# Kernel optimization log

Hardware: AMD Instinct MI355X
Metric: run time of the kernel (lower is better)

The kernel has to match this reference:

```python
import jax, jax.numpy as jnp
import numpy as np

GRID_SIZE = 8
POS_LAMBDA = 250.0
POS_MARGIN = 1.0
NEG_MARGIN = 0.2


def setup_inputs() -> dict:
    key = jax.random.key(0)
    k1, k2, k3, k4 = jax.random.split(key, 4)
    N, C, Hr, Wr = 8, 128, 30, 40
    H, W = Hr * GRID_SIZE, Wr * GRID_SIZE
    des1 = jax.random.normal(k1, (N, C, Hr, Wr), jnp.float32)
    des2 = jax.random.normal(k2, (N, C, Hr, Wr), jnp.float32)
    # near-identity homography so the positive-pair mask s is non-trivial
    homo = jnp.eye(3, dtype=jnp.float32) + 0.001 * jax.random.normal(k3, (3, 3), jnp.float32)
    mask = (jax.random.uniform(k4, (N, 1, H, W)) > 0.05).astype(jnp.float32)
    return {"des1": des1, "des2": des2, "homo": homo, "mask": mask}


def reference(des1, des2, homo, mask):
    n, c, hr, wr = des1.shape
    gs = GRID_SIZE

    # coordinate grid of cell centers in full-res pixel coords: (x, y)
    ys, xs = jnp.meshgrid(jnp.arange(hr), jnp.arange(wr), indexing='ij')
    grid = jnp.stack([xs, ys], axis=-1).astype(homo.dtype) * gs + gs // 2  # Hr,Wr,2
    grid = jnp.broadcast_to(grid, (n, hr, wr, 2))

    # warp grid by homography
    gh = jnp.concatenate([grid, jnp.ones((n, hr, wr, 1), homo.dtype)], axis=-1)  # N,Hr,Wr,3
    wg = jnp.einsum('nhwk,jk->nhwj', gh, homo)
    w_grid = wg[..., :2] / wg[..., 2:3]  # N,Hr,Wr,2

    # pairwise distance between grid cells of img1 and warped cells of img2
    diff = grid[:, :, :, None, None, :] - w_grid[:, None, None, :, :, :]  # N,Hr,Wr,Hr,Wr,2
    grid_dist = jnp.sqrt(jnp.sum(diff * diff, axis=-1))                   # N,Hr,Wr,Hr,Wr
    s = (grid_dist <= gs - 0.5).astype(des1.dtype)

    # dense descriptor cross-correlation (contraction over channels)
    dot_des = jnp.einsum('ncij,nckl->nijkl', des1, des2)  # N,Hr,Wr,Hr,Wr

    pos_dist = jnp.maximum(POS_MARGIN - dot_des, 0.0)
    neg_dist = jnp.maximum(dot_des - NEG_MARGIN, 0.0)
    loss = POS_LAMBDA * s * pos_dist + (1.0 - s) * neg_dist

    # space_to_depth(mask, gs).prod(dim=1)
    m = mask.reshape(n, 1, hr, gs, wr, gs)
    r_mask = jnp.prod(m, axis=(1, 3, 5))            # N,Hr,Wr
    r_mask5 = r_mask.reshape(n, 1, 1, hr, wr)

    norm = hr * wr * jnp.sum(r_mask5)
    loss = jnp.sum(loss * r_mask5) / norm
    return (loss, s, dot_des, r_mask5[:, 0])  # r_mask squeezed -> N,1,Hr,Wr
```

## Files before the change

kernel.cpp:

```cpp
#include <hip/hip_runtime.h>
#include <hip/hip_bf16.h>

#define HRr 30
#define WRr 40
#define MM 1200
#define CC 128
#define NB 8
#define GS 8

constexpr int PT = 19;
constexpr int TILE_SH = 16 * 64 * 8;
constexpr int NPART = 1200;

typedef __attribute__((ext_vector_type(8))) short bf16x8;
typedef __attribute__((ext_vector_type(4))) float f32x4;

__device__ inline short f2bf(float f) {
    union { float f; unsigned u; } v; v.f = f;
    unsigned r = v.u + 0x7FFFu + ((v.u >> 16) & 1u);
    return (short)(r >> 16);
}

__global__ __launch_bounds__(256) void convert_prep_kernel(const float* __restrict__ des1,
                                                           const float* __restrict__ des2,
                                                           const float* __restrict__ homo,
                                                           const float* __restrict__ mask,
                                                           short* __restrict__ wsA,
                                                           short* __restrict__ wsB,
                                                           float2* __restrict__ wgrid,
                                                           float* __restrict__ out_rmask,
                                                           float* __restrict__ ws_rmask) {
    const int t     = threadIdx.x;
    const int ptile = blockIdx.x;
    const int n     = blockIdx.z;

    if (blockIdx.y == 0) {
        const int gid = (blockIdx.z * gridDim.x + blockIdx.x) * 256 + t;
        if (gid < MM) {
            int k = gid / WRr, l = gid % WRr;
            float x = (float)(l * GS + GS / 2);
            float y = (float)(k * GS + GS / 2);
            float nx = homo[0] * x + homo[1] * y + homo[2];
            float ny = homo[3] * x + homo[4] * y + homo[5];
            float dn = homo[6] * x + homo[7] * y + homo[8];
            wgrid[gid] = make_float2(nx / dn, ny / dn);
        }
        if (gid < NB * MM) {
            int nn = gid / MM;
            int rem = gid % MM;
            int k = rem / WRr, l = rem % WRr;
            const float* mp = mask + (size_t)nn * (240 * 320) + (size_t)(k * GS) * 320 + l * GS;
            float prod = 1.f;
            #pragma unroll
            for (int yy = 0; yy < GS; ++yy) {
                float4 a = *reinterpret_cast<const float4*>(&mp[yy * 320]);
                float4 b = *reinterpret_cast<const float4*>(&mp[yy * 320 + 4]);
                prod *= a.x * a.y * a.z * a.w * b.x * b.y * b.z * b.w;
            }
            out_rmask[gid] = prod;
            ws_rmask[gid]  = prod;
        }
    }

    const int j = t & 63;
    const int g = t >> 6;
    const int p = ptile * 64 + j;

    const float* A = des1 + (size_t)n * CC * MM;
    const float* B = des2 + (size_t)n * CC * MM;
    short* outA = wsA + (size_t)(n * PT + ptile) * TILE_SH;
    short* outB = wsB + (size_t)(n * PT + ptile) * TILE_SH;

    const int rb = j >> 4, lc = j & 15;
    const int kr = blockIdx.y * 4 + g;
    const int kb = kr * 8;
    bf16x8 wa, wb;
    #pragma unroll
    for (int i = 0; i < 8; ++i) {
        float va = (p < MM) ? A[(size_t)(kb + i) * MM + p] : 0.f;
        float vb = (p < MM) ? B[(size_t)(kb + i) * MM + p] : 0.f;
        wa[i] = f2bf(va);
        wb[i] = f2bf(vb);
    }
    const int ks = kr >> 2, lr = kr & 3;
    const size_t off = (size_t)(((ks * 4 + rb) * 64) + lr * 16 + lc) * 8;
    *reinterpret_cast<bf16x8*>(&outA[off]) = wa;
    *reinterpret_cast<bf16x8*>(&outB[off]) = wb;
}

__global__ __launch_bounds__(256) void main_kernel(const short* __restrict__ wsA,
                                                   const short* __restrict__ wsB,
                                                   const float2* __restrict__ wgrid,
                                                   const float* __restrict__ rmask,
                                                   float* __restrict__ out_s,
                                                   float* __restrict__ out_dot,
                                                   float* __restrict__ partials) {
    __shared__ float Ds[16 * 612];
    __shared__ float red[4];

    const int f   = blockIdx.x;
    const int lid = (f & 7) * 150 + (f >> 3);
    const int n     = lid / 150;
    const int rem   = lid % 150;
    const int strip = rem >> 1;
    const int half  = rem & 1;
    const int p0    = strip * 16;
    const int cbase = half ? 608 : 0;
    const int nf    = half ? 37  : 38;
    const int W     = half ? 592 : 608;
    const int fbase = half ? 38  : 0;

    const int t    = threadIdx.x;
    const int lane = t & 63;
    const int w    = t >> 6;
    const int lr   = lane >> 4, lc = lane & 15;

    const short* An  = wsA + (size_t)(n * PT + (p0 >> 6)) * TILE_SH;
    const int    rbA = (p0 >> 4) & 3;
    bf16x8 af[4];
    #pragma unroll
    for (int ks = 0; ks < 4; ++ks)
        af[ks] = *reinterpret_cast<const bf16x8*>(&An[(size_t)(((ks * 4 + rbA) * 64) + lane) * 8]);

    const short* Bn = wsB + (size_t)n * PT * TILE_SH;
    const float* rm = rmask + n * MM;

    for (int i = w; i < nf; i += 4) {
        const int g = fbase + i;
        const short* Bt = Bn + (size_t)(g >> 2) * TILE_SH;
        const int rbB = g & 3;
        f32x4 acc = {0.f, 0.f, 0.f, 0.f};
        #pragma unroll
        for (int ks = 0; ks < 4; ++ks) {
            bf16x8 bfr = *reinterpret_cast<const bf16x8*>(
                &Bt[(size_t)(((ks * 4 + rbB) * 64) + lane) * 8]);
            acc = __builtin_amdgcn_mfma_f32_16x16x32_bf16(af[ks], bfr, acc, 0, 0, 0);
        }
        #pragma unroll
        for (int r = 0; r < 4; ++r)
            Ds[(lr * 4 + r) * 612 + 1 + i * 16 + lc] = acc[r];
    }
    __syncthreads();

    const int row = t >> 4;
    const int l16 = t & 15;
    const int p   = p0 + row;
    const float gx = (float)((p % WRr) * GS + GS / 2);
    const float gy = (float)((p / WRr) * GS + GS / 2);
    const size_t rowbase = (size_t)(n * MM + p) * MM;
    const int h = 31 - 16 * (p & 1);

    float lsum = 0.f;

    for (int c = l16; c < h; c += 16) {
        const float dot = Ds[row * 612 + 1 + c];
        const int q = cbase + c;
        const float2 wg = wgrid[q];
        const float dx = gx - wg.x, dy = gy - wg.y;
        const float dist = sqrtf(dx * dx + dy * dy);
        const float s = (dist <= 7.5f) ? 1.f : 0.f;
        const float le = 250.f * s * fmaxf(1.f - dot, 0.f) + (1.f - s) * fmaxf(dot - 0.2f, 0.f);
        lsum += le * rm[q];
        out_dot[rowbase + q] = dot;
        out_s[rowbase + q] = s;
    }
    const int nl = (W - h) >> 5;
    const int s4 = nl << 3;
    const int ts = h + (nl << 5);
    for (int k = 0;; ++k) {
        const int jj = l16 + (k << 4);
        if (jj >= s4) break;
        const int c = h + (jj << 2);
        const int q = cbase + c;
        const float4 dv = *reinterpret_cast<const float4*>(&Ds[row * 612 + 1 + c]);
        float sv[4];
        const float dd[4] = {dv.x, dv.y, dv.z, dv.w};
        #pragma unroll
        for (int u = 0; u < 4; ++u) {
            const float2 wg = wgrid[q + u];
            const float dx = gx - wg.x, dy = gy - wg.y;
            const float dist = sqrtf(dx * dx + dy * dy);
            const float s = (dist <= 7.5f) ? 1.f : 0.f;
            sv[u] = s;
            const float le = 250.f * s * fmaxf(1.f - dd[u], 0.f) + (1.f - s) * fmaxf(dd[u] - 0.2f, 0.f);
            lsum += le * rm[q + u];
        }
        *reinterpret_cast<float4*>(&out_dot[rowbase + q]) = dv;
        *reinterpret_cast<float4*>(&out_s[rowbase + q]) = make_float4(sv[0], sv[1], sv[2], sv[3]);
    }
    for (int c = ts + l16; c < W; c += 16) {
        const float dot = Ds[row * 612 + 1 + c];
        const int q = cbase + c;
        const float2 wg = wgrid[q];
        const float dx = gx - wg.x, dy = gy - wg.y;
        const float dist = sqrtf(dx * dx + dy * dy);
        const float s = (dist <= 7.5f) ? 1.f : 0.f;
        const float le = 250.f * s * fmaxf(1.f - dot, 0.f) + (1.f - s) * fmaxf(dot - 0.2f, 0.f);
        lsum += le * rm[q];
        out_dot[rowbase + q] = dot;
        out_s[rowbase + q] = s;
    }

    #pragma unroll
    for (int off = 32; off > 0; off >>= 1)
        lsum += __shfl_xor(lsum, off, 64);
    if (lane == 0) red[w] = lsum;
    __syncthreads();
    if (t == 0)
        partials[lid] = (red[0] + red[1]) + (red[2] + red[3]);
}

__global__ __launch_bounds__(1024) void final_kernel(const float* __restrict__ partials,
                                                     const float* __restrict__ rmask,
                                                     float* __restrict__ out_loss) {
    __shared__ float red[1024];
    const int t = threadIdx.x;

    float s1 = 0.f;
    for (int i = t; i < NPART; i += 1024) s1 += partials[i];
    red[t] = s1;
    __syncthreads();
    for (int off = 512; off > 0; off >>= 1) {
        if (t < off) red[t] += red[t + off];
        __syncthreads();
    }
    float total = red[0];
    __syncthreads();

    float s2 = 0.f;
    for (int i = t; i < NB * MM; i += 1024) s2 += rmask[i];
    red[t] = s2;
    __syncthreads();
    for (int off = 512; off > 0; off >>= 1) {
        if (t < off) red[t] += red[t + off];
        __syncthreads();
    }
    if (t == 0) out_loss[0] = total / ((float)MM * red[0]);
}

extern "C" void kernel_launch(void* const* d_in, const int* in_sizes, int n_in,
                              void* d_out, int out_size, void* d_ws, size_t ws_size,
                              hipStream_t stream) {
    const float* des1 = (const float*)d_in[0];
    const float* des2 = (const float*)d_in[1];
    const float* homo = (const float*)d_in[2];
    const float* mask = (const float*)d_in[3];

    float* out      = (float*)d_out;
    float* out_loss = out;
    float* out_s    = out + 1;
    float* out_dot  = out + 1 + (size_t)NB * MM * MM;
    float* out_rm   = out + 1 + 2 * (size_t)NB * MM * MM;

    char* wsb = (char*)d_ws;
    float2* wgrid    = (float2*)(wsb);
    float*  partials = (float*)(wsb + 16384);
    float*  ws_rm    = (float*)(wsb + 32768);
    short*  wsA      = (short*)(wsb + 131072);
    short*  wsB      = wsA + (size_t)NB * PT * TILE_SH;

    dim3 cgrid(PT, 4, NB);
    convert_prep_kernel<<<cgrid, 256, 0, stream>>>(des1, des2, homo, mask,
                                                   wsA, wsB, wgrid, out_rm, ws_rm);

    main_kernel<<<dim3(NPART, 1, 1), 256, 0, stream>>>(wsA, wsB, wgrid, ws_rm,
                                                       out_s, out_dot, partials);

    final_kernel<<<1, 1024, 0, stream>>>(partials, ws_rm, out_loss);
}
```

Measured before the change: 46.53 us.

## Overlap MFMA fragment compute with epilogue stores, use nontemporal stores, warp-reduce final

```diff
diff --git a/kernel.cpp b/kernel.cpp
--- a/kernel.cpp
+++ b/kernel.cpp
@@ -125,7 +125,7 @@
     const short* Bn = wsB + (size_t)n * PT * TILE_SH;
     const float* rm = rmask + n * MM;
 
-    for (int i = w; i < nf; i += 4) {
+    auto do_frag = [&](int i) {
         const int g = fbase + i;
         const short* Bt = Bn + (size_t)(g >> 2) * TILE_SH;
         const int rbB = g & 3;
@@ -139,8 +139,7 @@
         #pragma unroll
         for (int r = 0; r < 4; ++r)
             Ds[(lr * 4 + r) * 612 + 1 + i * 16 + lc] = acc[r];
-    }
-    __syncthreads();
+    };
 
     const int row = t >> 4;
     const int l16 = t & 15;
@@ -152,7 +151,7 @@
 
     float lsum = 0.f;
 
-    for (int c = l16; c < h; c += 16) {
+    auto emit_scalar = [&](int c) {
         const float dot = Ds[row * 612 + 1 + c];
         const int q = cbase + c;
         const float2 wg = wgrid[q];
@@ -161,45 +160,49 @@
         const float s = (dist <= 7.5f) ? 1.f : 0.f;
         const float le = 250.f * s * fmaxf(1.f - dot, 0.f) + (1.f - s) * fmaxf(dot - 0.2f, 0.f);
         lsum += le * rm[q];
-        out_dot[rowbase + q] = dot;
-        out_s[rowbase + q] = s;
-    }
-    const int nl = (W - h) >> 5;
-    const int s4 = nl << 3;
-    const int ts = h + (nl << 5);
-    for (int k = 0;; ++k) {
-        const int jj = l16 + (k << 4);
-        if (jj >= s4) break;
-        const int c = h + (jj << 2);
-        const int q = cbase + c;
-        const float4 dv = *reinterpret_cast<const float4*>(&Ds[row * 612 + 1 + c]);
-        float sv[4];
-        const float dd[4] = {dv.x, dv.y, dv.z, dv.w};
-        #pragma unroll
-        for (int u = 0; u < 4; ++u) {
-            const float2 wg = wgrid[q + u];
-            const float dx = gx - wg.x, dy = gy - wg.y;
-            const float dist = sqrtf(dx * dx + dy * dy);
-            const float s = (dist <= 7.5f) ? 1.f : 0.f;
-            sv[u] = s;
-            const float le = 250.f * s * fmaxf(1.f - dd[u], 0.f) + (1.f - s) * fmaxf(dd[u] - 0.2f, 0.f);
-            lsum += le * rm[q + u];
-        }
-        *reinterpret_cast<float4*>(&out_dot[rowbase + q]) = dv;
-        *reinterpret_cast<float4*>(&out_s[rowbase + q]) = make_float4(sv[0], sv[1], sv[2], sv[3]);
-    }
-    for (int c = ts + l16; c < W; c += 16) {
-        const float dot = Ds[row * 612 + 1 + c];
-        const int q = cbase + c;
-        const float2 wg = wgrid[q];
-        const float dx = gx - wg.x, dy = gy - wg.y;
-        const float dist = sqrtf(dx * dx + dy * dy);
-        const float s = (dist <= 7.5f) ? 1.f : 0.f;
-        const float le = 250.f * s * fmaxf(1.f - dot, 0.f) + (1.f - s) * fmaxf(dot - 0.2f, 0.f);
-        lsum += le * rm[q];
-        out_dot[rowbase + q] = dot;
-        out_s[rowbase + q] = s;
-    }
+        __builtin_nontemporal_store(dot, &out_dot[rowbase + q]);
+        __builtin_nontemporal_store(s, &out_s[rowbase + q]);
+    };
+
+    auto emit_range = [&](int cLo, int cHi) {
+        int cAl = cLo + (((h - cLo) % 32) + 32) % 32;
+        if (cAl > cHi) cAl = cHi;
+        for (int c = cLo + l16; c < cAl; c += 16) emit_scalar(c);
+        const int nl = (cHi - cAl) >> 5;
+        const int s4 = nl << 3;
+        const int cTs = cAl + (nl << 5);
+        for (int k = 0;; ++k) {
+            const int jj = l16 + (k << 4);
+            if (jj >= s4) break;
+            const int c = cAl + (jj << 2);
+            const int q = cbase + c;
+            const f32x4 dv = *reinterpret_cast<const f32x4*>(&Ds[row * 612 + 1 + c]);
+            f32x4 sv;
+            #pragma unroll
+            for (int u = 0; u < 4; ++u) {
+                const float2 wg = wgrid[q + u];
+                const float dx = gx - wg.x, dy = gy - wg.y;
+                const float dist = sqrtf(dx * dx + dy * dy);
+                const float s = (dist <= 7.5f) ? 1.f : 0.f;
+                sv[u] = s;
+                const float le = 250.f * s * fmaxf(1.f - dv[u], 0.f) + (1.f - s) * fmaxf(dv[u] - 0.2f, 0.f);
+                lsum += le * rm[q + u];
+            }
+            __builtin_nontemporal_store(dv, reinterpret_cast<f32x4*>(&out_dot[rowbase + q]));
+            __builtin_nontemporal_store(sv, reinterpret_cast<f32x4*>(&out_s[rowbase + q]));
+        }
+        for (int c = cTs + l16; c < cHi; c += 16) emit_scalar(c);
+    };
+
+    for (int i = w; i < 20; i += 4) do_frag(i);
+    __syncthreads();
+
+    for (int i = 20 + w; i < nf; i += 4) do_frag(i);
+    const int c_split = h + 288;
+    emit_range(0, c_split);
+    __syncthreads();
+
+    emit_range(c_split, W);
 
     #pragma unroll
     for (int off = 32; off > 0; off >>= 1)
@@ -213,29 +216,27 @@
 __global__ __launch_bounds__(1024) void final_kernel(const float* __restrict__ partials,
                                                      const float* __restrict__ rmask,
                                                      float* __restrict__ out_loss) {
-    __shared__ float red[1024];
+    __shared__ float r1[16], r2[16];
     const int t = threadIdx.x;
-
-    float s1 = 0.f;
+    const int lane = t & 63;
+    const int w = t >> 6;
+
+    float s1 = 0.f, s2 = 0.f;
     for (int i = t; i < NPART; i += 1024) s1 += partials[i];
-    red[t] = s1;
-    __syncthreads();
-    for (int off = 512; off > 0; off >>= 1) {
-        if (t < off) red[t] += red[t + off];
-        __syncthreads();
-    }
-    float total = red[0];
-    __syncthreads();
-
-    float s2 = 0.f;
     for (int i = t; i < NB * MM; i += 1024) s2 += rmask[i];
-    red[t] = s2;
-    __syncthreads();
-    for (int off = 512; off > 0; off >>= 1) {
-        if (t < off) red[t] += red[t + off];
-        __syncthreads();
-    }
-    if (t == 0) out_loss[0] = total / ((float)MM * red[0]);
+    #pragma unroll
+    for (int off = 32; off > 0; off >>= 1) {
+        s1 += __shfl_xor(s1, off, 64);
+        s2 += __shfl_xor(s2, off, 64);
+    }
+    if (lane == 0) { r1[w] = s1; r2[w] = s2; }
+    __syncthreads();
+    if (t == 0) {
+        float total = 0.f, rsum = 0.f;
+        #pragma unroll
+        for (int i = 0; i < 16; ++i) { total += r1[i]; rsum += r2[i]; }
+        out_loss[0] = total / ((float)MM * rsum);
+    }
 }
 
 extern "C" void kernel_launch(void* const* d_in, const int* in_sizes, int n_in,
```

Result: slower. 48.33 us (+3.8%).
